# Performance work log

Measured on AMD Instinct MI355X. Metric: run time of the kernel, lower is better.

## Reference

```python
import jax, jax.numpy as jnp
import numpy as np

B, L, D, H = 4, 2048, 256, 512


def silu_backward(x):
    s = jax.nn.silu(x)
    return s + jax.nn.sigmoid(x) * (1.0 - s)


def setup_inputs() -> dict:
    key = jax.random.key(0)
    ks = jax.random.split(key, 12)
    sc = 0.02
    return {
        "x": jax.random.normal(ks[0], (B, L, D), jnp.float32),
        "W1": jax.random.normal(ks[1], (B, H, D), jnp.float32) * sc,
        "W2": jax.random.normal(ks[2], (B, D, H), jnp.float32) * sc,
        "Wq": jax.random.normal(ks[3], (D, D), jnp.float32) * sc,
        "bq": jnp.zeros((D,), jnp.float32),
        "Wk": jax.random.normal(ks[4], (D, D), jnp.float32) * sc,
        "bk": jnp.zeros((D,), jnp.float32),
        "Wv": jax.random.normal(ks[5], (D, D), jnp.float32) * sc,
        "bv": jnp.zeros((D,), jnp.float32),
        "w_lr": jax.random.normal(ks[6], (D,), jnp.float32) * sc,
        "b_lr": jnp.zeros((), jnp.float32),
        "w_wd": jax.random.normal(ks[7], (D,), jnp.float32) * sc,
        "b_wd": jnp.zeros((), jnp.float32),
        "log_base_lr": jnp.asarray(np.log(0.1), jnp.float32),
        "log_base_wd": jnp.asarray(np.log(0.5), jnp.float32),
    }


def reference(x, W1, W2, Wq, bq, Wk, bk, Wv, bv, w_lr, b_lr, w_wd, b_wd, log_base_lr, log_base_wd):
    b, l, d = x.shape
    query = x @ Wq + bq
    key = x @ Wk + bk
    value = x @ Wv + bv
    lr = jnp.exp(log_base_lr) * jax.nn.sigmoid(x @ w_lr + b_lr)          # [b,l]
    log_wd = jnp.log(1.0 - jnp.exp(log_base_wd) * jax.nn.sigmoid(x @ w_wd + b_wd))  # [b,l]

    wd_cross = jnp.exp(jnp.cumsum(log_wd, axis=1))                       # [b,l]
    idx = jnp.arange(l)
    strict_upper = idx[:, None] < idx[None, :]                           # (m, j): j > m
    A = jnp.where(strict_upper[None], log_wd[:, None, :], 0.0)           # [b,m,j]
    wd_inner = jnp.exp(jnp.cumsum(A, axis=2)) * (idx[:, None] <= idx[None, :])[None]  # [b,m,j]

    X1 = key
    Z1 = jnp.einsum('bhd,bld->blh', W1, X1)
    X2 = jax.nn.silu(Z1)
    Z2 = jnp.einsum('bdh,blh->bld', W2, X2)
    grad_Z2 = Z2 - value
    grad_X2 = jnp.einsum('bdh,bld->blh', W2, grad_Z2)
    grad_Z1 = silu_backward(Z1) * grad_X2

    X1_ = query
    mask_X1X1_ = jnp.einsum('bld,bmd->blm', X1, X1_) * wd_inner
    Z1_inner = -jnp.einsum('blh,bl,blm->bmh', grad_Z1, lr, mask_X1X1_)
    Z1_cross = jnp.einsum('bhd,bld,bl->blh', W1, X1_, wd_cross)
    Z1_ = Z1_inner + Z1_cross

    W1_next = (-jnp.einsum('blh,bl,bld->bhd', grad_Z1, lr * wd_inner[:, :, -1], X1)
               + W1 * wd_cross[:, -1][:, None, None])

    X2_ = jax.nn.silu(Z1_)
    mask_X2X2_ = jnp.einsum('blh,bmh->blm', X2, X2_) * wd_inner
    Z2_inner = -jnp.einsum('bld,bl,blm->bmd', grad_Z2, lr, mask_X2X2_)
    Z2_cross = jnp.einsum('bdh,blh,bl->bld', W2, X2_, wd_cross)
    Z2_ = Z2_inner + Z2_cross

    W2_next = (-jnp.einsum('bld,bl,blh->bdh', grad_Z2, lr * wd_inner[:, :, -1], X2)
               + W2 * wd_cross[:, -1][:, None, None])

    return (Z2_, W1_next, W2_next)
```

## Files before the change

kernel.cpp:

```cpp
#include <hip/hip_runtime.h>

typedef __bf16 bf16;
typedef __bf16 bf16x8 __attribute__((ext_vector_type(8)));
typedef __bf16 bf16x4 __attribute__((ext_vector_type(4)));
typedef float  f32x4  __attribute__((ext_vector_type(4)));

#define SB 72
#define CUTOFF -18.0

__device__ __forceinline__ float silu_f(float x){
  float s = 1.f/(1.f+__expf(-x));
  return x*s;
}
__device__ __forceinline__ float silu_bwd_f(float x){
  float s = 1.f/(1.f+__expf(-x));
  float si = x*s;
  return si + s*(1.f-si);
}

struct MArgs {
  const bf16* A; const bf16* B;
  long sA, sB;
  int lda, ldb;
  int M, N, K;
  int mode;
  float* Cf; long sCf;
  bf16*  Cb; long sCb;
  bf16*  Cb2; long sCb2;
  bf16*  Ct;  long sCt;  int ldct;
  int ldc;
  const float* auxf; int ldax; long sAuxf;
  const bf16*  auxb; long sAuxb;
  const float* rowv; long sRowv;
  const double* cd;  long sCd;
  const float* ks;   long sKs;
  const float* clp;  long sClp;
  bf16* Q; bf16* Ko; float* Vo; const float* bqkv;
};

template<int TM>
__device__ __forceinline__ void gemm_body(const MArgs& g, int bm, int bn, int bz)
{
  const int row0 = bm*TM, col0 = bn*64;
  constexpr int NI  = TM/32;
  constexpr int TPR = 256/TM;
  constexpr int EPR = 64/TPR;
  constexpr int NCH = EPR/8;

  const bf16* A = g.A + (long)bz*g.sA;
  const bf16* B = g.B + (long)bz*g.sB;
  const float* ksp = g.ks ? g.ks + (long)bz*g.sKs : (const float*)0;
  const double* cd = g.cd ? g.cd + (long)bz*g.sCd : (const double*)0;
  float* Cf = g.Cf ? g.Cf + (long)bz*g.sCf : (float*)0;
  bf16* Cb  = g.Cb ? g.Cb + (long)bz*g.sCb : (bf16*)0;
  bf16* Cb2 = g.Cb2 ? g.Cb2 + (long)bz*g.sCb2 : (bf16*)0;
  bf16* Ct  = g.Ct ? g.Ct + (long)bz*g.sCt : (bf16*)0;
  const float* auxf = g.auxf ? g.auxf + (long)bz*g.sAuxf : (const float*)0;
  const bf16*  auxb = g.auxb ? g.auxb + (long)bz*g.sAuxb : (const bf16*)0;
  const float* rowv = g.rowv ? g.rowv + (long)bz*g.sRowv : (const float*)0;

  const int tid = threadIdx.x;
  const int mode = g.mode;
  const int lane = tid & 63;
  const int w = tid >> 6;
  const int wr = (w >> 1) * (TM/2), wc = (w & 1) * 32;
  const int l15 = lane & 15;
  const int quad = lane >> 4;

  __shared__ __align__(16) bf16 As[TM*SB];
  __shared__ __align__(16) bf16 Bs[64*SB];

  f32x4 acc[NI][2];
  #pragma unroll
  for (int i=0;i<NI;i++)
    #pragma unroll
    for (int j=0;j<2;j++)
      #pragma unroll
      for (int r=0;r<4;r++) acc[i][j][r] = 0.f;

  const int rowA = tid / TPR, kA = (tid % TPR) * EPR;
  const int rowB = tid >> 2,  kB = (tid & 3) * 16;

  int klo = 0;
  if (cd && ksp) {
    const double cref = cd[g.K-1];
    while (klo + 64 < g.K && (cref - cd[klo+63]) < CUTOFF) klo += 64;
  }

  for (int k0 = klo; k0 < g.K; k0 += 64) {
    {
      const bf16* s = A + (long)(row0+rowA)*g.lda + k0 + kA;
      bf16x8 v[NCH];
      #pragma unroll
      for (int p=0;p<NCH;p++) v[p] = *(const bf16x8*)(s + p*8);
      if (ksp) {
        #pragma unroll
        for (int p=0;p<NCH;p++)
          #pragma unroll
          for (int i=0;i<8;i++)
            v[p][i] = (bf16)((float)v[p][i] * ksp[k0+kA+p*8+i]);
      }
      #pragma unroll
      for (int p=0;p<NCH;p++) *(bf16x8*)&As[rowA*SB + kA + p*8] = v[p];
    }
    {
      const bf16* s = B + (long)(col0+rowB)*g.ldb + k0 + kB;
      *(bf16x8*)&Bs[rowB*SB + kB]     = *(const bf16x8*)s;
      *(bf16x8*)&Bs[rowB*SB + kB + 8] = *(const bf16x8*)(s+8);
    }
    __syncthreads();
    #pragma unroll
    for (int ch=0; ch<2; ch++){
      bf16x8 af[NI], bf2[2];
      #pragma unroll
      for (int i=0;i<NI;i++) af[i]  = *(const bf16x8*)&As[(wr + i*16 + l15)*SB + ch*32 + quad*8];
      #pragma unroll
      for (int j=0;j<2;j++) bf2[j] = *(const bf16x8*)&Bs[(wc + j*16 + l15)*SB + ch*32 + quad*8];
      #pragma unroll
      for (int i=0;i<NI;i++)
        #pragma unroll
        for (int j=0;j<2;j++)
          acc[i][j] = __builtin_amdgcn_mfma_f32_16x16x32_bf16(af[i], bf2[j], acc[i][j], 0, 0, 0);
    }
    __syncthreads();
  }

  float clv = 0.f;
  if (mode == 10) clv = *(g.clp + (long)bz*g.sClp);

  #pragma unroll
  for (int i=0;i<NI;i++){
    const int rb = row0 + wr + i*16 + quad*4;
    #pragma unroll
    for (int j=0;j<2;j++){
      const int c = col0 + wc + j*16 + l15;
      bf16 tv[4]; bool doT = false;
      #pragma unroll
      for (int reg=0; reg<4; reg++){
        const int r = rb + reg;
        float v = acc[i][j][reg];
        const long co = (long)r*g.ldc + c;
        switch (mode) {
          case 1: {
            Cb[co]  = (bf16)v;
            bf16 sv = (bf16)silu_f(v);
            Cb2[co] = sv;
            tv[reg] = sv; doT = true;
          } break;
          case 2: {
            bf16 o = (bf16)(v - auxf[(long)r*g.ldax + c]);
            Cb[co] = o; tv[reg] = o; doT = true;
          } break;
          case 3: {
            bf16 o = (bf16)(silu_bwd_f((float)auxb[(long)r*g.ldax + c]) * v * rowv[r]);
            Cb[co] = o; tv[reg] = o; doT = true;
          } break;
          case 10: {
            Cf[co] = v + auxf[(long)r*g.ldax + c]*clv;
          } break;
          case 11: {
            float o = v + g.bqkv[c];
            if (c < 256)      g.Q [(long)r*256 + c]       = (bf16)o;
            else if (c < 512) { g.Ko[(long)r*256 + (c-256)] = (bf16)o; tv[reg] = (bf16)o; doT = true; }
            else              g.Vo[(long)r*256 + (c-512)] = o;
          } break;
        }
      }
      if (doT && Ct) {
        bf16x4 t4 = { tv[0], tv[1], tv[2], tv[3] };
        if (mode == 11) {
          const int b = rb / g.ldct, l = rb % g.ldct;
          *(bf16x4*)&Ct[(long)b*g.sCt + (long)(c-256)*g.ldct + l] = t4;
        } else {
          *(bf16x4*)&Ct[(long)c*g.ldct + rb] = t4;
        }
      }
    }
  }
}

__global__ __launch_bounds__(256)
void mfma_gemm128(MArgs g){ gemm_body<128>(g, blockIdx.x, blockIdx.y, blockIdx.z); }

__global__ __launch_bounds__(256)
void mfma_gemm64(MArgs g){ gemm_body<64>(g, blockIdx.x, blockIdx.y, blockIdx.z); }

__global__ __launch_bounds__(256)
void wnext_gemm(MArgs g1, MArgs g2){
  const int z = blockIdx.z;
  const MArgs& g = (z < 4) ? g1 : g2;
  const int bz = z & 3;
  if ((int)blockIdx.x*128 >= g.M || (int)blockIdx.y*64 >= g.N) return;
  gemm_body<128>(g, blockIdx.x, blockIdx.y, bz);
}

struct PArgs {
  const bf16 *A, *B1;
  long sA, sB1;
  const double* cd; long sCd;
  const float* lrv; long sLr;
  bf16* P;
};

template<int KS64, int ISLR>
__global__ __launch_bounds__(256)
void pgen(PArgs g)
{
  const int mt = blockIdx.x, slot = blockIdx.y, bz = blockIdx.z;
  const int m0 = mt*64;
  const int l0 = (m0 & ~127) - slot*128;
  if (l0 < 0) return;
  const double* cd = g.cd + (long)bz*g.sCd;
  const int lref = (l0+127 < m0) ? (l0+127) : m0;
  if (cd[m0] - cd[lref] < CUTOFF) return;

  const int K1 = KS64*64;
  const bf16* A  = g.A  + (long)bz*g.sA;
  const bf16* B1 = g.B1 + (long)bz*g.sB1;
  const float* lrv = ISLR ? (g.lrv + (long)bz*g.sLr) : (const float*)0;

  const int tid = threadIdx.x;
  const int lane = tid & 63, w = tid >> 6;
  const int wr = (w>>1)*32, wc = (w&1)*64;
  const int l15 = lane & 15, quad = lane >> 4;
  const int rowA = tid >> 2, kA = (tid & 3) * 16;
  const int rowB = tid >> 1, kB = (tid & 1) * 32;

  __shared__ __align__(16) bf16 As[64*SB];
  __shared__ __align__(16) bf16 Bs[128*SB];

  f32x4 O[2][4];
  #pragma unroll
  for (int i=0;i<2;i++)
    #pragma unroll
    for (int j=0;j<4;j++)
      #pragma unroll
      for (int r=0;r<4;r++) O[i][j][r] = 0.f;

  for (int ks=0; ks<KS64; ks++){
    const int k0 = ks*64;
    {
      const bf16* s = A + (long)(m0+rowA)*K1 + k0 + kA;
      *(bf16x8*)&As[rowA*SB + kA]     = *(const bf16x8*)s;
      *(bf16x8*)&As[rowA*SB + kA + 8] = *(const bf16x8*)(s+8);
    }
    {
      const bf16* s = B1 + (long)(l0+rowB)*K1 + k0 + kB;
      #pragma unroll
      for (int p=0;p<4;p++) *(bf16x8*)&Bs[rowB*SB + kB + p*8] = *(const bf16x8*)(s + p*8);
    }
    __syncthreads();
    #pragma unroll
    for (int ch=0; ch<2; ch++){
      bf16x8 af[2], bfr[4];
      #pragma unroll
      for (int i=0;i<2;i++) af[i]  = *(const bf16x8*)&As[(wr + i*16 + l15)*SB + ch*32 + quad*8];
      #pragma unroll
      for (int j=0;j<4;j++) bfr[j] = *(const bf16x8*)&Bs[(wc + j*16 + l15)*SB + ch*32 + quad*8];
      #pragma unroll
      for (int i=0;i<2;i++)
        #pragma unroll
        for (int j=0;j<4;j++)
          O[i][j] = __builtin_amdgcn_mfma_f32_16x16x32_bf16(af[i], bfr[j], O[i][j], 0, 0, 0);
    }
    __syncthreads();
  }

  bf16* Pt = g.P + (((long)bz*32 + mt)*3 + slot) * (64*128);
  float cl[4], lv[4];
  #pragma unroll
  for (int j=0;j<4;j++){
    const int l = l0 + wc + j*16 + l15;
    cl[j] = (float)cd[l];
    if (ISLR) lv[j] = lrv[l];
  }
  #pragma unroll
  for (int i=0;i<2;i++)
    #pragma unroll
    for (int reg=0; reg<4; reg++){
      const int mloc = wr + i*16 + quad*4 + reg;
      const int m = m0 + mloc;
      const float cm = (float)cd[m];
      #pragma unroll
      for (int j=0;j<4;j++){
        const int lloc = wc + j*16 + l15;
        const int l = l0 + lloc;
        float v = -O[i][j][reg] * __expf(cm - cl[j]);
        if (ISLR) v *= lv[j];
        if (l > m) v = 0.f;
        Pt[mloc*128 + lloc] = (bf16)v;
      }
    }
}

struct CArgs {
  const bf16 *A, *W, *P, *B2;
  long sA, sW, sB2;
  int ldb2;
  const double* cd; long sCd;
  const float* wdc; long sWdc;
  float* Cf; long sCf;
  bf16* Cb; long sCb;
  int ldc;
};

template<int KS64, int SILU, int ZSPLIT>
__global__ __launch_bounds__(256)
void cons(CArgs g)
{
  const int mt = blockIdx.x;
  const int m0 = mt*64, n0 = blockIdx.y*128;
  const int bz   = ZSPLIT ? (blockIdx.z >> 1) : blockIdx.z;
  const int half = ZSPLIT ? (blockIdx.z & 1)  : 0;
  const int K1 = KS64*64;
  const bf16* A  = g.A  + (long)bz*g.sA;
  const bf16* W  = g.W  + (long)bz*g.sW;
  const bf16* B2 = g.B2 + (long)bz*g.sB2;
  const double* cd = g.cd + (long)bz*g.sCd;
  const float* wdc = g.wdc + (long)bz*g.sWdc;

  const int tid = threadIdx.x;
  const int lane = tid & 63, w = tid >> 6;
  const int wr = (w>>1)*32, wc = (w&1)*64;
  const int l15 = lane & 15, quad = lane >> 4;
  const int rowA = tid >> 2, kA = (tid & 3) * 16;
  const int rowB = tid >> 1, kB = (tid & 1) * 32;

  bool alive[3];
  int nalive = 0;
  #pragma unroll
  for (int s=0;s<3;s++){
    const int l0 = (m0 & ~127) - s*128;
    bool a = (l0 >= 0);
    if (a) {
      const int lref = (l0+127 < m0) ? (l0+127) : m0;
      a = (cd[m0] - cd[lref] >= CUTOFF);
    }
    alive[s] = a; nalive += a ? 1 : 0;
  }
  if (ZSPLIT && half == 1 && nalive == 0) return;

  __shared__ __align__(16) bf16 As[64*SB];
  __shared__ __align__(16) bf16 Bs[128*SB];

  f32x4 O[2][4];
  #pragma unroll
  for (int i=0;i<2;i++)
    #pragma unroll
    for (int j=0;j<4;j++)
      #pragma unroll
      for (int r=0;r<4;r++) O[i][j][r] = 0.f;

  if (half == 0) {
    for (int ks=0; ks<KS64; ks++){
      const int k0 = ks*64;
      {
        const bf16* s = A + (long)(m0+rowA)*K1 + k0 + kA;
        *(bf16x8*)&As[rowA*SB + kA]     = *(const bf16x8*)s;
        *(bf16x8*)&As[rowA*SB + kA + 8] = *(const bf16x8*)(s+8);
      }
      {
        const bf16* s = W + (long)(n0+rowB)*K1 + k0 + kB;
        #pragma unroll
        for (int p=0;p<4;p++) *(bf16x8*)&Bs[rowB*SB + kB + p*8] = *(const bf16x8*)(s + p*8);
      }
      __syncthreads();
      #pragma unroll
      for (int ch=0; ch<2; ch++){
        bf16x8 af[2], bfr[4];
        #pragma unroll
        for (int i=0;i<2;i++) af[i]  = *(const bf16x8*)&As[(wr + i*16 + l15)*SB + ch*32 + quad*8];
        #pragma unroll
        for (int j=0;j<4;j++) bfr[j] = *(const bf16x8*)&Bs[(wc + j*16 + l15)*SB + ch*32 + quad*8];
        #pragma unroll
        for (int i=0;i<2;i++)
          #pragma unroll
          for (int j=0;j<4;j++)
            O[i][j] = __builtin_amdgcn_mfma_f32_16x16x32_bf16(af[i], bfr[j], O[i][j], 0, 0, 0);
      }
      __syncthreads();
    }
    #pragma unroll
    for (int i=0;i<2;i++)
      #pragma unroll
      for (int reg=0; reg<4; reg++){
        const float s = wdc[m0 + wr + i*16 + quad*4 + reg];
        #pragma unroll
        for (int j=0;j<4;j++) O[i][j][reg] *= s;
      }
  }

  if (!ZSPLIT || half == 1) {
    for (int s=0; s<3; s++){
      if (!alive[s]) continue;
      const int l0 = (m0 & ~127) - s*128;
      const bf16* Pt = g.P + (((long)bz*32 + mt)*3 + s) * (64*128);
      for (int hk=0; hk<2; hk++){
        {
          const bf16* sp = Pt + (long)rowA*128 + hk*64 + kA;
          *(bf16x8*)&As[rowA*SB + kA]     = *(const bf16x8*)sp;
          *(bf16x8*)&As[rowA*SB + kA + 8] = *(const bf16x8*)(sp+8);
        }
        {
          const bf16* sp = B2 + (long)(n0+rowB)*g.ldb2 + l0 + hk*64 + kB;
          #pragma unroll
          for (int p=0;p<4;p++) *(bf16x8*)&Bs[rowB*SB + kB + p*8] = *(const bf16x8*)(sp + p*8);
        }
        __syncthreads();
        #pragma unroll
        for (int ch=0; ch<2; ch++){
          bf16x8 af[2], bfr[4];
          #pragma unroll
          for (int i=0;i<2;i++) af[i]  = *(const bf16x8*)&As[(wr + i*16 + l15)*SB + ch*32 + quad*8];
          #pragma unroll
          for (int j=0;j<4;j++) bfr[j] = *(const bf16x8*)&Bs[(wc + j*16 + l15)*SB + ch*32 + quad*8];
          #pragma unroll
          for (int i=0;i<2;i++)
            #pragma unroll
            for (int j=0;j<4;j++)
              O[i][j] = __builtin_amdgcn_mfma_f32_16x16x32_bf16(af[i], bfr[j], O[i][j], 0, 0, 0);
        }
        __syncthreads();
      }
    }
  }

  #pragma unroll
  for (int i=0;i<2;i++){
    const int rb = m0 + wr + i*16 + quad*4;
    #pragma unroll
    for (int j=0;j<4;j++){
      const int c = n0 + wc + j*16 + l15;
      #pragma unroll
      for (int reg=0; reg<4; reg++){
        const long co = (long)(rb+reg)*g.ldc + c;
        if (ZSPLIT)     unsafeAtomicAdd(&g.Cf[(long)bz*g.sCf + co], O[i][j][reg]);
        else if (SILU)  g.Cb[(long)bz*g.sCb + co] = (bf16)silu_f(O[i][j][reg]);
        else            g.Cf[(long)bz*g.sCf + co] = O[i][j][reg];
      }
    }
  }
}

__global__ __launch_bounds__(256)
void conv_multi(const float* __restrict__ a, bf16* __restrict__ oa, long na,
                const float* __restrict__ b, bf16* __restrict__ ob, long nb,
                const float* __restrict__ c, bf16* __restrict__ oc, long nc)
{
  const int job = blockIdx.y;
  const float* src = job==0 ? a : (job==1 ? b : c);
  bf16* dst       = job==0 ? oa : (job==1 ? ob : oc);
  const long n    = job==0 ? na : (job==1 ? nb : nc);
  long i = ((long)blockIdx.x*256 + threadIdx.x)*8;
  if (i >= n) return;
  float4 x = *(const float4*)&src[i];
  float4 y = *(const float4*)&src[i+4];
  bf16x8 o;
  o[0]=(bf16)x.x; o[1]=(bf16)x.y; o[2]=(bf16)x.z; o[3]=(bf16)x.w;
  o[4]=(bf16)y.x; o[5]=(bf16)y.y; o[6]=(bf16)y.z; o[7]=(bf16)y.w;
  *(bf16x8*)&dst[i] = o;
}

__global__ __launch_bounds__(256)
void transpose_multi(const float* __restrict__ Wq, const float* __restrict__ Wk,
                     const float* __restrict__ Wv, bf16* __restrict__ Wqkvt,
                     const float* __restrict__ W2, bf16* __restrict__ W2t, long HD)
{
  __shared__ bf16 t[64][72];
  const int z = blockIdx.z;
  const float* ip; bf16* op; int R, C;
  if (z < 3) {
    if (blockIdx.y >= 4) return;
    ip = z==0 ? Wq : (z==1 ? Wk : Wv);
    op = Wqkvt + (long)z*256*256;
    R = 256; C = 256;
  } else {
    ip = W2 + (long)(z-3)*HD;
    op = W2t + (long)(z-3)*HD;
    R = 256; C = 512;
  }
  const int r0 = blockIdx.x*64, c0 = blockIdx.y*64;
  const int tid = threadIdx.x;
  const int lr_ = tid>>2, lc = (tid&3)*16;
  #pragma unroll
  for (int q=0;q<4;q++){
    float4 a = *(const float4*)&ip[(long)(r0+lr_)*C + c0+lc + q*4];
    t[lr_][lc+q*4+0] = (bf16)a.x; t[lr_][lc+q*4+1] = (bf16)a.y;
    t[lr_][lc+q*4+2] = (bf16)a.z; t[lr_][lc+q*4+3] = (bf16)a.w;
  }
  __syncthreads();
  const int oc = tid>>2, orr = (tid&3)*16;
  bf16x8 u, v;
  #pragma unroll
  for (int i=0;i<8;i++){ u[i] = t[orr+i][oc]; v[i] = t[orr+8+i][oc]; }
  *(bf16x8*)&op[(long)(c0+oc)*R + r0+orr]   = u;
  *(bf16x8*)&op[(long)(c0+oc)*R + r0+orr+8] = v;
}

__global__ __launch_bounds__(256)
void scalar_proj_kernel(const float* __restrict__ x,
                        const float* __restrict__ wlr, const float* __restrict__ blr,
                        const float* __restrict__ wwd, const float* __restrict__ bwd,
                        const float* __restrict__ lbl, const float* __restrict__ lbw,
                        float* __restrict__ lr, float* __restrict__ lw)
{
  const int row  = blockIdx.x*4 + (threadIdx.x >> 6);
  const int lane = threadIdx.x & 63;
  const float4 a = ((const float4*)(x + (long)row*256))[lane];
  const float4 u = ((const float4*)wlr)[lane];
  const float4 w = ((const float4*)wwd)[lane];
  float d1 = a.x*u.x + a.y*u.y + a.z*u.z + a.w*u.w;
  float d2 = a.x*w.x + a.y*w.y + a.z*w.z + a.w*w.w;
  #pragma unroll
  for (int off=32; off; off>>=1) {
    d1 += __shfl_down(d1, off);
    d2 += __shfl_down(d2, off);
  }
  if (lane == 0) {
    float s1 = 1.f/(1.f+expf(-(d1 + blr[0])));
    lr[row] = expf(lbl[0]) * s1;
    float s2 = 1.f/(1.f+expf(-(d2 + bwd[0])));
    lw[row] = logf(1.f - expf(lbw[0]) * s2);
  }
}

__global__ __launch_bounds__(256)
void cumsum_kernel(const float* __restrict__ lw, const float* __restrict__ lr,
                   double* __restrict__ cd, float* __restrict__ wdc,
                   float* __restrict__ se1, float* __restrict__ se2, int L,
                   const float* __restrict__ bq, const float* __restrict__ bk,
                   const float* __restrict__ bv, float* __restrict__ bqkv)
{
  const int b = blockIdx.x;
  const int t = threadIdx.x;
  if (b == 4) {
    for (int i = t; i < 768; i += 256)
      bqkv[i] = (i<256) ? bq[i] : ((i<512) ? bk[i-256] : bv[i-512]);
    return;
  }
  const float* lwb = lw + (long)b*L;
  __shared__ double sum_s[256];
  double loc[8];
  double s = 0.0;
  #pragma unroll
  for (int i=0;i<8;i++){ s += (double)lwb[t*8+i]; loc[i] = s; }
  sum_s[t] = s;
  __syncthreads();
  for (int off=1; off<256; off<<=1){
    double v = 0.0;
    if (t >= off) v = sum_s[t-off];
    __syncthreads();
    sum_s[t] += v;
    __syncthreads();
  }
  const double prefix = (t > 0) ? sum_s[t-1] : 0.0;
  const double total  = sum_s[255];
  #pragma unroll
  for (int i=0;i<8;i++){
    double c = prefix + loc[i];
    long idx = (long)b*L + t*8 + i;
    cd[idx]  = c;
    wdc[idx] = (float)exp(c);
    double e = exp(total - c);
    se1[idx] = (float)(-e);
    se2[idx] = (float)(-e) * lr[idx];
  }
}

extern "C" void kernel_launch(void* const* d_in, const int* in_sizes, int n_in,
                              void* d_out, int out_size, void* d_ws, size_t ws_size,
                              hipStream_t stream)
{
  const int Bn = 4, L = 2048, D = 256, H = 512;
  const long LD = (long)L*D, LH = (long)L*H, HD = (long)H*D;

  const float* x   = (const float*)d_in[0];
  const float* W1  = (const float*)d_in[1];
  const float* W2  = (const float*)d_in[2];
  const float* Wq  = (const float*)d_in[3];
  const float* bq  = (const float*)d_in[4];
  const float* Wk  = (const float*)d_in[5];
  const float* bk  = (const float*)d_in[6];
  const float* Wv  = (const float*)d_in[7];
  const float* bv  = (const float*)d_in[8];
  const float* wlr = (const float*)d_in[9];
  const float* blr = (const float*)d_in[10];
  const float* wwd = (const float*)d_in[11];
  const float* bwd = (const float*)d_in[12];
  const float* lbl = (const float*)d_in[13];
  const float* lbw = (const float*)d_in[14];
  (void)in_sizes; (void)n_in; (void)out_size; (void)ws_size;

  float* out0 = (float*)d_out;
  float* out1 = out0 + (long)Bn*LD;
  float* out2 = out1 + (long)Bn*HD;

  char* wsp = (char*)d_ws;
  size_t off = 0;
  auto alloc = [&](size_t bytes)->void*{
    void* p = wsp + off; off += (bytes + 255) & ~(size_t)255; return p;
  };
  bf16* xb    = (bf16*)alloc((size_t)Bn*LD*2);
  bf16* Wqkvt = (bf16*)alloc((size_t)3*D*D*2);
  float* bqkv = (float*)alloc((size_t)3*D*4);
  bf16* W1b  = (bf16*)alloc((size_t)Bn*HD*2);
  bf16* W2b  = (bf16*)alloc((size_t)Bn*HD*2);
  bf16* W2t  = (bf16*)alloc((size_t)Bn*HD*2);
  bf16* Qb   = (bf16*)alloc((size_t)Bn*LD*2);
  bf16* Kb   = (bf16*)alloc((size_t)Bn*LD*2);
  bf16* Kt   = (bf16*)alloc((size_t)Bn*LD*2);
  float* Vf  = (float*)alloc((size_t)Bn*LD*4);
  bf16* Z1b  = (bf16*)alloc((size_t)Bn*LH*2);
  bf16* X2b  = (bf16*)alloc((size_t)Bn*LH*2);
  bf16* X2t  = (bf16*)alloc((size_t)Bn*LH*2);
  bf16* gZb  = (bf16*)alloc((size_t)Bn*LD*2);
  bf16* gZt  = (bf16*)alloc((size_t)Bn*LD*2);
  bf16* A1b  = (bf16*)alloc((size_t)Bn*LH*2);
  bf16* A1t  = (bf16*)alloc((size_t)Bn*LH*2);
  bf16* X2_b = (bf16*)alloc((size_t)Bn*LH*2);
  bf16* Pb1  = (bf16*)alloc((size_t)Bn*32*3*64*128*2);
  bf16* Pb2  = (bf16*)alloc((size_t)Bn*32*3*64*128*2);
  float* lrb = (float*)alloc((size_t)Bn*L*4);
  float* lwb = (float*)alloc((size_t)Bn*L*4);
  float* wdc = (float*)alloc((size_t)Bn*L*4);
  float* se1 = (float*)alloc((size_t)Bn*L*4);
  float* se2 = (float*)alloc((size_t)Bn*L*4);
  double* cdb = (double*)alloc((size_t)Bn*L*8);

  auto run128 = [&](const MArgs& g, int Z){
    dim3 grid(g.M/128, g.N/64, Z);
    mfma_gemm128<<<grid, 256, 0, stream>>>(g);
  };
  auto run64 = [&](const MArgs& g, int Z){
    dim3 grid(g.M/64, g.N/64, Z);
    mfma_gemm64<<<grid, 256, 0, stream>>>(g);
  };

  hipMemsetAsync(out0, 0, (size_t)Bn*LD*4, stream);

  conv_multi<<<dim3(1024,3), 256, 0, stream>>>(x, xb, Bn*LD, W1, W1b, Bn*HD, W2, W2b, Bn*HD);
  transpose_multi<<<dim3(4,8,7), 256, 0, stream>>>(Wq, Wk, Wv, Wqkvt, W2, W2t, HD);
  scalar_proj_kernel<<<dim3(Bn*L/4), 256, 0, stream>>>(x, wlr, blr, wwd, bwd, lbl, lbw, lrb, lwb);
  cumsum_kernel<<<dim3(5), 256, 0, stream>>>(lwb, lrb, cdb, wdc, se1, se2, L, bq, bk, bv, bqkv);

  {
    MArgs g{}; g.A = xb; g.lda = D; g.B = Wqkvt; g.ldb = D;
    g.M = Bn*L; g.N = 3*D; g.K = D; g.mode = 11; g.ldc = 0;
    g.Q = Qb; g.Ko = Kb; g.Vo = Vf; g.bqkv = bqkv;
    g.Ct = Kt; g.sCt = LD; g.ldct = L;
    run128(g, 1);
  }
  {
    MArgs g{}; g.A = Kb; g.lda = D; g.sA = LD; g.B = W1b; g.ldb = D; g.sB = HD;
    g.M = L; g.N = H; g.K = D; g.mode = 1; g.ldc = H;
    g.Cb = Z1b; g.sCb = LH; g.Cb2 = X2b; g.sCb2 = LH;
    g.Ct = X2t; g.sCt = LH; g.ldct = L; run64(g, Bn);
  }
  {
    MArgs g{}; g.A = X2b; g.lda = H; g.sA = LH; g.B = W2b; g.ldb = H; g.sB = HD;
    g.M = L; g.N = D; g.K = H; g.mode = 2; g.ldc = D;
    g.auxf = Vf; g.ldax = D; g.sAuxf = LD; g.Cb = gZb; g.sCb = LD;
    g.Ct = gZt; g.sCt = LD; g.ldct = L; run64(g, Bn);
  }
  {
    MArgs g{}; g.A = gZb; g.lda = D; g.sA = LD; g.B = W2t; g.ldb = D; g.sB = HD;
    g.M = L; g.N = H; g.K = D; g.mode = 3; g.ldc = H;
    g.auxb = Z1b; g.ldax = H; g.sAuxb = LH; g.rowv = lrb; g.sRowv = L;
    g.Cb = A1b; g.sCb = LH;
    g.Ct = A1t; g.sCt = LH; g.ldct = L; run64(g, Bn);
  }
  {
    PArgs p{};
    p.A = Qb; p.sA = LD; p.B1 = Kb; p.sB1 = LD;
    p.cd = cdb; p.sCd = L; p.P = Pb1;
    pgen<4,0><<<dim3(32,3,Bn), 256, 0, stream>>>(p);
  }
  {
    CArgs c{};
    c.A = Qb; c.sA = LD; c.W = W1b; c.sW = HD;
    c.P = Pb1; c.B2 = A1t; c.sB2 = LH; c.ldb2 = L;
    c.cd = cdb; c.sCd = L; c.wdc = wdc; c.sWdc = L;
    c.Cb = X2_b; c.sCb = LH; c.ldc = H;
    cons<4,1,0><<<dim3(32, H/128, Bn), 256, 0, stream>>>(c);
  }
  {
    PArgs p{};
    p.A = X2_b; p.sA = LH; p.B1 = X2b; p.sB1 = LH;
    p.cd = cdb; p.sCd = L; p.lrv = lrb; p.sLr = L; p.P = Pb2;
    pgen<8,1><<<dim3(32,3,Bn), 256, 0, stream>>>(p);
  }
  {
    CArgs c{};
    c.A = X2_b; c.sA = LH; c.W = W2b; c.sW = HD;
    c.P = Pb2; c.B2 = gZt; c.sB2 = LD; c.ldb2 = L;
    c.cd = cdb; c.sCd = L; c.wdc = wdc; c.sWdc = L;
    c.Cf = out0; c.sCf = LD; c.ldc = D;
    cons<8,0,1><<<dim3(32, D/128, Bn*2), 256, 0, stream>>>(c);
  }
  {
    MArgs g1{}; g1.A = A1t; g1.lda = L; g1.sA = LH; g1.B = Kt; g1.ldb = L; g1.sB = LD;
    g1.M = H; g1.N = D; g1.K = L; g1.mode = 10; g1.ldc = D;
    g1.ks = se1; g1.sKs = L; g1.cd = cdb; g1.sCd = L;
    g1.auxf = W1; g1.ldax = D; g1.sAuxf = HD; g1.clp = wdc + (L-1); g1.sClp = L;
    g1.Cf = out1; g1.sCf = HD;

    MArgs g2{}; g2.A = gZt; g2.lda = L; g2.sA = LD; g2.B = X2t; g2.ldb = L; g2.sB = LH;
    g2.M = D; g2.N = H; g2.K = L; g2.mode = 10; g2.ldc = H;
    g2.ks = se2; g2.sKs = L; g2.cd = cdb; g2.sCd = L;
    g2.auxf = W2; g2.ldax = H; g2.sAuxf = HD; g2.clp = wdc + (L-1); g2.sClp = L;
    g2.Cf = out2; g2.sCf = HD;

    wnext_gemm<<<dim3(4,8,8), 256, 0, stream>>>(g1, g2);
  }
}
```

Measured before the change: 240.7 us.

## Merge independent launches into combined front, A1+pgen1, and pgen2+wnext kernels

```diff
diff --git a/kernel.cpp b/kernel.cpp
--- a/kernel.cpp
+++ b/kernel.cpp
@@ -39,7 +39,8 @@
 };
 
 template<int TM>
-__device__ __forceinline__ void gemm_body(const MArgs& g, int bm, int bn, int bz)
+__device__ __forceinline__ void gemm_body(const MArgs& g, int bm, int bn, int bz,
+                                          bf16* As, bf16* Bs)
 {
   const int row0 = bm*TM, col0 = bn*64;
   constexpr int NI  = TM/32;
@@ -66,9 +67,6 @@
   const int wr = (w >> 1) * (TM/2), wc = (w & 1) * 32;
   const int l15 = lane & 15;
   const int quad = lane >> 4;
-
-  __shared__ __align__(16) bf16 As[TM*SB];
-  __shared__ __align__(16) bf16 Bs[64*SB];
 
   f32x4 acc[NI][2];
   #pragma unroll
@@ -180,18 +178,15 @@
 }
 
 __global__ __launch_bounds__(256)
-void mfma_gemm128(MArgs g){ gemm_body<128>(g, blockIdx.x, blockIdx.y, blockIdx.z); }
+void mfma_gemm128(MArgs g){
+  __shared__ __align__(16) bf16 smem[(128+64)*SB];
+  gemm_body<128>(g, blockIdx.x, blockIdx.y, blockIdx.z, smem, smem + 128*SB);
+}
 
 __global__ __launch_bounds__(256)
-void mfma_gemm64(MArgs g){ gemm_body<64>(g, blockIdx.x, blockIdx.y, blockIdx.z); }
-
-__global__ __launch_bounds__(256)
-void wnext_gemm(MArgs g1, MArgs g2){
-  const int z = blockIdx.z;
-  const MArgs& g = (z < 4) ? g1 : g2;
-  const int bz = z & 3;
-  if ((int)blockIdx.x*128 >= g.M || (int)blockIdx.y*64 >= g.N) return;
-  gemm_body<128>(g, blockIdx.x, blockIdx.y, bz);
+void mfma_gemm64(MArgs g){
+  __shared__ __align__(16) bf16 smem[(64+64)*SB];
+  gemm_body<64>(g, blockIdx.x, blockIdx.y, blockIdx.z, smem, smem + 64*SB);
 }
 
 struct PArgs {
@@ -203,10 +198,9 @@
 };
 
 template<int KS64, int ISLR>
-__global__ __launch_bounds__(256)
-void pgen(PArgs g)
+__device__ __forceinline__ void pgen_body(const PArgs& g, int mt, int slot, int bz,
+                                          bf16* As, bf16* Bs)
 {
-  const int mt = blockIdx.x, slot = blockIdx.y, bz = blockIdx.z;
   const int m0 = mt*64;
   const int l0 = (m0 & ~127) - slot*128;
   if (l0 < 0) return;
@@ -225,9 +219,6 @@
   const int l15 = lane & 15, quad = lane >> 4;
   const int rowA = tid >> 2, kA = (tid & 3) * 16;
   const int rowB = tid >> 1, kB = (tid & 1) * 32;
-
-  __shared__ __align__(16) bf16 As[64*SB];
-  __shared__ __align__(16) bf16 Bs[128*SB];
 
   f32x4 O[2][4];
   #pragma unroll
@@ -291,6 +282,34 @@
         Pt[mloc*128 + lloc] = (bf16)v;
       }
     }
+}
+
+__global__ __launch_bounds__(256)
+void a1_pgen1(MArgs ga, PArgs gp){
+  __shared__ __align__(16) bf16 smem[192*SB];
+  const int z = blockIdx.z;
+  if (z < 4) {
+    gemm_body<64>(ga, blockIdx.x, blockIdx.y, z, smem, smem + 64*SB);
+  } else {
+    if (blockIdx.y >= 3) return;
+    pgen_body<4,0>(gp, blockIdx.x, blockIdx.y, z - 4, smem, smem + 64*SB);
+  }
+}
+
+__global__ __launch_bounds__(256)
+void pgen2_wnext(PArgs gp, MArgs g1, MArgs g2){
+  __shared__ __align__(16) bf16 smem[192*SB];
+  const int z = blockIdx.z;
+  if (z < 4) {
+    if (blockIdx.y >= 3) return;
+    pgen_body<8,1>(gp, blockIdx.x, blockIdx.y, z, smem, smem + 64*SB);
+  } else {
+    const int z2 = z - 4;
+    const MArgs& g = (z2 < 4) ? g1 : g2;
+    const int bz = z2 & 3;
+    if ((int)blockIdx.x*128 >= g.M || (int)blockIdx.y*64 >= g.N) return;
+    gemm_body<128>(g, blockIdx.x, blockIdx.y, bz, smem, smem + 128*SB);
+  }
 }
 
 struct CArgs {
@@ -442,85 +461,96 @@
   }
 }
 
+struct FrontArgs {
+  const float *x, *W1, *W2, *Wq, *Wk, *Wv;
+  bf16 *xb, *W1b, *W2b, *Wqkvt, *W2t;
+  float* out0;
+  const float *wlr, *blr, *wwd, *bwd, *lbl, *lbw;
+  float *lr, *lw;
+  long LD4, HD4, HD;
+};
+
 __global__ __launch_bounds__(256)
-void conv_multi(const float* __restrict__ a, bf16* __restrict__ oa, long na,
-                const float* __restrict__ b, bf16* __restrict__ ob, long nb,
-                const float* __restrict__ c, bf16* __restrict__ oc, long nc)
-{
-  const int job = blockIdx.y;
-  const float* src = job==0 ? a : (job==1 ? b : c);
-  bf16* dst       = job==0 ? oa : (job==1 ? ob : oc);
-  const long n    = job==0 ? na : (job==1 ? nb : nc);
-  long i = ((long)blockIdx.x*256 + threadIdx.x)*8;
-  if (i >= n) return;
-  float4 x = *(const float4*)&src[i];
-  float4 y = *(const float4*)&src[i+4];
-  bf16x8 o;
-  o[0]=(bf16)x.x; o[1]=(bf16)x.y; o[2]=(bf16)x.z; o[3]=(bf16)x.w;
-  o[4]=(bf16)y.x; o[5]=(bf16)y.y; o[6]=(bf16)y.z; o[7]=(bf16)y.w;
-  *(bf16x8*)&dst[i] = o;
-}
-
-__global__ __launch_bounds__(256)
-void transpose_multi(const float* __restrict__ Wq, const float* __restrict__ Wk,
-                     const float* __restrict__ Wv, bf16* __restrict__ Wqkvt,
-                     const float* __restrict__ W2, bf16* __restrict__ W2t, long HD)
+void front_kernel(FrontArgs f)
 {
   __shared__ bf16 t[64][72];
-  const int z = blockIdx.z;
-  const float* ip; bf16* op; int R, C;
-  if (z < 3) {
-    if (blockIdx.y >= 4) return;
-    ip = z==0 ? Wq : (z==1 ? Wk : Wv);
-    op = Wqkvt + (long)z*256*256;
-    R = 256; C = 256;
-  } else {
-    ip = W2 + (long)(z-3)*HD;
-    op = W2t + (long)(z-3)*HD;
-    R = 256; C = 512;
-  }
-  const int r0 = blockIdx.x*64, c0 = blockIdx.y*64;
+  const int bid = blockIdx.x;
   const int tid = threadIdx.x;
-  const int lr_ = tid>>2, lc = (tid&3)*16;
-  #pragma unroll
-  for (int q=0;q<4;q++){
-    float4 a = *(const float4*)&ip[(long)(r0+lr_)*C + c0+lc + q*4];
-    t[lr_][lc+q*4+0] = (bf16)a.x; t[lr_][lc+q*4+1] = (bf16)a.y;
-    t[lr_][lc+q*4+2] = (bf16)a.z; t[lr_][lc+q*4+3] = (bf16)a.w;
-  }
-  __syncthreads();
-  const int oc = tid>>2, orr = (tid&3)*16;
-  bf16x8 u, v;
-  #pragma unroll
-  for (int i=0;i<8;i++){ u[i] = t[orr+i][oc]; v[i] = t[orr+8+i][oc]; }
-  *(bf16x8*)&op[(long)(c0+oc)*R + r0+orr]   = u;
-  *(bf16x8*)&op[(long)(c0+oc)*R + r0+orr+8] = v;
-}
-
-__global__ __launch_bounds__(256)
-void scalar_proj_kernel(const float* __restrict__ x,
-                        const float* __restrict__ wlr, const float* __restrict__ blr,
-                        const float* __restrict__ wwd, const float* __restrict__ bwd,
-                        const float* __restrict__ lbl, const float* __restrict__ lbw,
-                        float* __restrict__ lr, float* __restrict__ lw)
-{
-  const int row  = blockIdx.x*4 + (threadIdx.x >> 6);
-  const int lane = threadIdx.x & 63;
-  const float4 a = ((const float4*)(x + (long)row*256))[lane];
-  const float4 u = ((const float4*)wlr)[lane];
-  const float4 w = ((const float4*)wwd)[lane];
-  float d1 = a.x*u.x + a.y*u.y + a.z*u.z + a.w*u.w;
-  float d2 = a.x*w.x + a.y*w.y + a.z*w.z + a.w*w.w;
-  #pragma unroll
-  for (int off=32; off; off>>=1) {
-    d1 += __shfl_down(d1, off);
-    d2 += __shfl_down(d2, off);
-  }
-  if (lane == 0) {
-    float s1 = 1.f/(1.f+expf(-(d1 + blr[0])));
-    lr[row] = expf(lbl[0]) * s1;
-    float s2 = 1.f/(1.f+expf(-(d2 + bwd[0])));
-    lw[row] = logf(1.f - expf(lbw[0]) * s2);
+
+  if (bid < 1536) {
+    const float* src; bf16* dst; long n; long base;
+    if (bid < 1024)      { src = f.x;  dst = f.xb;  n = f.LD4; base = (long)bid*2048; }
+    else if (bid < 1280) { src = f.W1; dst = f.W1b; n = f.HD4; base = (long)(bid-1024)*2048; }
+    else                 { src = f.W2; dst = f.W2b; n = f.HD4; base = (long)(bid-1280)*2048; }
+    long i = base + (long)tid*8;
+    if (i >= n) return;
+    float4 a = *(const float4*)&src[i];
+    float4 b = *(const float4*)&src[i+4];
+    bf16x8 o;
+    o[0]=(bf16)a.x; o[1]=(bf16)a.y; o[2]=(bf16)a.z; o[3]=(bf16)a.w;
+    o[4]=(bf16)b.x; o[5]=(bf16)b.y; o[6]=(bf16)b.z; o[7]=(bf16)b.w;
+    *(bf16x8*)&dst[i] = o;
+    return;
+  }
+  if (bid < 2560) {
+    long i = (long)(bid-1536)*2048 + (long)tid*8;
+    float4 z = {0.f,0.f,0.f,0.f};
+    *(float4*)&f.out0[i]   = z;
+    *(float4*)&f.out0[i+4] = z;
+    return;
+  }
+  if (bid < 2736) {
+    const float* ip; bf16* op; int R, C; int r0, c0;
+    if (bid < 2608) {
+      const int r = bid - 2560;
+      const int z = r >> 4, rem = r & 15;
+      ip = z==0 ? f.Wq : (z==1 ? f.Wk : f.Wv);
+      op = f.Wqkvt + (long)z*256*256;
+      R = 256; C = 256;
+      r0 = (rem & 3)*64; c0 = (rem >> 2)*64;
+    } else {
+      const int r = bid - 2608;
+      const int b = r >> 5, rem = r & 31;
+      ip = f.W2 + (long)b*f.HD;
+      op = f.W2t + (long)b*f.HD;
+      R = 256; C = 512;
+      r0 = (rem & 3)*64; c0 = (rem >> 2)*64;
+    }
+    const int lr_ = tid>>2, lc = (tid&3)*16;
+    #pragma unroll
+    for (int q=0;q<4;q++){
+      float4 a = *(const float4*)&ip[(long)(r0+lr_)*C + c0+lc + q*4];
+      t[lr_][lc+q*4+0] = (bf16)a.x; t[lr_][lc+q*4+1] = (bf16)a.y;
+      t[lr_][lc+q*4+2] = (bf16)a.z; t[lr_][lc+q*4+3] = (bf16)a.w;
+    }
+    __syncthreads();
+    const int oc = tid>>2, orr = (tid&3)*16;
+    bf16x8 u, v;
+    #pragma unroll
+    for (int i=0;i<8;i++){ u[i] = t[orr+i][oc]; v[i] = t[orr+8+i][oc]; }
+    *(bf16x8*)&op[(long)(c0+oc)*R + r0+orr]   = u;
+    *(bf16x8*)&op[(long)(c0+oc)*R + r0+orr+8] = v;
+    return;
+  }
+  {
+    const int row  = (bid-2736)*4 + (tid >> 6);
+    const int lane = tid & 63;
+    const float4 a = ((const float4*)(f.x + (long)row*256))[lane];
+    const float4 u = ((const float4*)f.wlr)[lane];
+    const float4 w = ((const float4*)f.wwd)[lane];
+    float d1 = a.x*u.x + a.y*u.y + a.z*u.z + a.w*u.w;
+    float d2 = a.x*w.x + a.y*w.y + a.z*w.z + a.w*w.w;
+    #pragma unroll
+    for (int off=32; off; off>>=1) {
+      d1 += __shfl_down(d1, off);
+      d2 += __shfl_down(d2, off);
+    }
+    if (lane == 0) {
+      float s1 = 1.f/(1.f+expf(-(d1 + f.blr[0])));
+      f.lr[row] = expf(f.lbl[0]) * s1;
+      float s2 = 1.f/(1.f+expf(-(d2 + f.bwd[0])));
+      f.lw[row] = logf(1.f - expf(f.lbw[0]) * s2);
+    }
   }
 }
 
@@ -636,11 +666,16 @@
     mfma_gemm64<<<grid, 256, 0, stream>>>(g);
   };
 
-  hipMemsetAsync(out0, 0, (size_t)Bn*LD*4, stream);
-
-  conv_multi<<<dim3(1024,3), 256, 0, stream>>>(x, xb, Bn*LD, W1, W1b, Bn*HD, W2, W2b, Bn*HD);
-  transpose_multi<<<dim3(4,8,7), 256, 0, stream>>>(Wq, Wk, Wv, Wqkvt, W2, W2t, HD);
-  scalar_proj_kernel<<<dim3(Bn*L/4), 256, 0, stream>>>(x, wlr, blr, wwd, bwd, lbl, lbw, lrb, lwb);
+  {
+    FrontArgs f{};
+    f.x = x; f.W1 = W1; f.W2 = W2; f.Wq = Wq; f.Wk = Wk; f.Wv = Wv;
+    f.xb = xb; f.W1b = W1b; f.W2b = W2b; f.Wqkvt = Wqkvt; f.W2t = W2t;
+    f.out0 = out0;
+    f.wlr = wlr; f.blr = blr; f.wwd = wwd; f.bwd = bwd; f.lbl = lbl; f.lbw = lbw;
+    f.lr = lrb; f.lw = lwb;
+    f.LD4 = Bn*LD; f.HD4 = Bn*HD; f.HD = HD;
+    front_kernel<<<dim3(4784), 256, 0, stream>>>(f);
+  }
   cumsum_kernel<<<dim3(5), 256, 0, stream>>>(lwb, lrb, cdb, wdc, se1, se2, L, bq, bk, bv, bqkv);
 
   {
@@ -663,17 +698,17 @@
     g.Ct = gZt; g.sCt = LD; g.ldct = L; run64(g, Bn);
   }
   {
-    MArgs g{}; g.A = gZb; g.lda = D; g.sA = LD; g.B = W2t; g.ldb = D; g.sB = HD;
-    g.M = L; g.N = H; g.K = D; g.mode = 3; g.ldc = H;
-    g.auxb = Z1b; g.ldax = H; g.sAuxb = LH; g.rowv = lrb; g.sRowv = L;
-    g.Cb = A1b; g.sCb = LH;
-    g.Ct = A1t; g.sCt = LH; g.ldct = L; run64(g, Bn);
-  }
-  {
-    PArgs p{};
-    p.A = Qb; p.sA = LD; p.B1 = Kb; p.sB1 = LD;
-    p.cd = cdb; p.sCd = L; p.P = Pb1;
-    pgen<4,0><<<dim3(32,3,Bn), 256, 0, stream>>>(p);
+    MArgs ga{}; ga.A = gZb; ga.lda = D; ga.sA = LD; ga.B = W2t; ga.ldb = D; ga.sB = HD;
+    ga.M = L; ga.N = H; ga.K = D; ga.mode = 3; ga.ldc = H;
+    ga.auxb = Z1b; ga.ldax = H; ga.sAuxb = LH; ga.rowv = lrb; ga.sRowv = L;
+    ga.Cb = A1b; ga.sCb = LH;
+    ga.Ct = A1t; ga.sCt = LH; ga.ldct = L;
+
+    PArgs gp{};
+    gp.A = Qb; gp.sA = LD; gp.B1 = Kb; gp.sB1 = LD;
+    gp.cd = cdb; gp.sCd = L; gp.P = Pb1;
+
+    a1_pgen1<<<dim3(32, 8, 8), 256, 0, stream>>>(ga, gp);
   }
   {
     CArgs c{};
@@ -684,10 +719,23 @@
     cons<4,1,0><<<dim3(32, H/128, Bn), 256, 0, stream>>>(c);
   }
   {
-    PArgs p{};
-    p.A = X2_b; p.sA = LH; p.B1 = X2b; p.sB1 = LH;
-    p.cd = cdb; p.sCd = L; p.lrv = lrb; p.sLr = L; p.P = Pb2;
-    pgen<8,1><<<dim3(32,3,Bn), 256, 0, stream>>>(p);
+    PArgs gp{};
+    gp.A = X2_b; gp.sA = LH; gp.B1 = X2b; gp.sB1 = LH;
+    gp.cd = cdb; gp.sCd = L; gp.lrv = lrb; gp.sLr = L; gp.P = Pb2;
+
+    MArgs g1{}; g1.A = A1t; g1.lda = L; g1.sA = LH; g1.B = Kt; g1.ldb = L; g1.sB = LD;
+    g1.M = H; g1.N = D; g1.K = L; g1.mode = 10; g1.ldc = D;
+    g1.ks = se1; g1.sKs = L; g1.cd = cdb; g1.sCd = L;
+    g1.auxf = W1; g1.ldax = D; g1.sAuxf = HD; g1.clp = wdc + (L-1); g1.sClp = L;
+    g1.Cf = out1; g1.sCf = HD;
+
+    MArgs g2{}; g2.A = gZt; g2.lda = L; g2.sA = LD; g2.B = X2t; g2.ldb = L; g2.sB = LH;
+    g2.M = D; g2.N = H; g2.K = L; g2.mode = 10; g2.ldc = H;
+    g2.ks = se2; g2.sKs = L; g2.cd = cdb; g2.sCd = L;
+    g2.auxf = W2; g2.ldax = H; g2.sAuxf = HD; g2.clp = wdc + (L-1); g2.sClp = L;
+    g2.Cf = out2; g2.sCf = HD;
+
+    pgen2_wnext<<<dim3(32, 8, 12), 256, 0, stream>>>(gp, g1, g2);
   }
   {
     CArgs c{};
@@ -697,19 +745,4 @@
     c.Cf = out0; c.sCf = LD; c.ldc = D;
     cons<8,0,1><<<dim3(32, D/128, Bn*2), 256, 0, stream>>>(c);
   }
-  {
-    MArgs g1{}; g1.A = A1t; g1.lda = L; g1.sA = LH; g1.B = Kt; g1.ldb = L; g1.sB = LD;
-    g1.M = H; g1.N = D; g1.K = L; g1.mode = 10; g1.ldc = D;
-    g1.ks = se1; g1.sKs = L; g1.cd = cdb; g1.sCd = L;
-    g1.auxf = W1; g1.ldax = D; g1.sAuxf = HD; g1.clp = wdc + (L-1); g1.sClp = L;
-    g1.Cf = out1; g1.sCf = HD;
-
-    MArgs g2{}; g2.A = gZt; g2.lda = L; g2.sA = LD; g2.B = X2t; g2.ldb = L; g2.sB = LH;
-    g2.M = D; g2.N = H; g2.K = L; g2.mode = 10; g2.ldc = H;
-    g2.ks = se2; g2.sKs = L; g2.cd = cdb; g2.sCd = L;
-    g2.auxf = W2; g2.ldax = H; g2.sAuxf = HD; g2.clp = wdc + (L-1); g2.sClp = L;
-    g2.Cf = out2; g2.sCf = HD;
-
-    wnext_gemm<<<dim3(4,8,8), 256, 0, stream>>>(g1, g2);
-  }
-}
+}
```

Measured after the change: 246.6 us. 2.5% more time.
